# Performance work log

Hardware: AMD Instinct MI355X
Metric: run time of the kernel (lower is better)

Reference implementation:

```python
import jax, jax.numpy as jnp
import numpy as np

EPS = 1e-12  # torch F.normalize eps


def _l2norm(x, axis):
    n = jnp.maximum(jnp.linalg.norm(x, axis=axis, keepdims=True), EPS)
    return x / n


def setup_inputs() -> dict:
    key = jax.random.key(0)
    k1, k2, k3, k4, k5 = jax.random.split(key, 5)
    N, E, IN_DIM, FAC_K, DIM_K = 100000, 1600000, 64, 4, 16
    all_emb = jax.random.normal(k1, (N, IN_DIM), dtype=jnp.float32) * 0.1
    W = jax.random.normal(k2, (FAC_K, IN_DIM, DIM_K), dtype=jnp.float32) * (1.0 / np.sqrt(IN_DIM))
    b = jax.random.normal(k3, (FAC_K, 1, DIM_K), dtype=jnp.float32) * 0.02
    row = jax.random.randint(k4, (E,), 0, N, dtype=jnp.int32)
    col = jax.random.randint(k5, (E,), 0, N, dtype=jnp.int32)
    return {"all_emb": all_emb, "W": W, "b": b, "row": row, "col": col, "iter_k": 2}


def reference(all_emb, W, b, row, col, iter_k):
    N = all_emb.shape[0]
    # factorized projection: [N, in_dim] x [K, in_dim, dk] -> [K, N, dk]
    fac = jnp.einsum('nd,kdf->knf', all_emb, W + b)
    fac = jax.nn.leaky_relu(fac, negative_slope=0.2)
    fac = _l2norm(fac, axis=2)

    new_fac = fac
    for _ in range(iter_k):
        head = new_fac[:, row]            # [K, E, dk]
        tail = fac[:, col]                # [K, E, dk]
        p_uv = jnp.sum(head * tail, axis=2)   # [K, E]
        p_uv = jax.nn.softmax(p_uv, axis=0)   # softmax over factors
        p_uv = jax.lax.stop_gradient(p_uv)    # original detaches attention
        msg = p_uv[:, :, None] * tail         # [K, E, dk]
        agg = jax.vmap(lambda m: jax.ops.segment_sum(m, row, num_segments=N))(msg)
        new_fac = _l2norm(fac + agg, axis=2)  # [K, N, dk]

    # torch.cat(list(new_fac_emb), dim=1) -> [N, K*dk]
    out = jnp.transpose(new_fac, (1, 0, 2)).reshape(N, -1)
    return out
```

## Files before the change

kernel.cpp:

```cpp
#include <hip/hip_runtime.h>

#define IN_DIM 64
#define FAC_K  4
#define DIM_K  16
#define SH     6
#define EPB    8192
#define CAP    2048

typedef _Float16 h2v __attribute__((ext_vector_type(2)));
typedef _Float16 h8v __attribute__((ext_vector_type(8)));
typedef float    f4v __attribute__((ext_vector_type(4)));

__device__ inline int   h2i(h2v v) { return __builtin_bit_cast(int, v); }
__device__ inline h2v   i2h(int v) { return __builtin_bit_cast(h2v, v); }
__device__ inline h2v   pkh(float a, float b) {
    return __builtin_bit_cast(h2v, __builtin_amdgcn_cvt_pkrtz(a, b));
}

#if __has_builtin(__builtin_amdgcn_fdot2)
__device__ inline float FDOT2(h2v a, h2v b, float c) {
    return __builtin_amdgcn_fdot2(a, b, c, false);
}
#else
__device__ inline float FDOT2(h2v a, h2v b, float c) {
    return c + (float)a.x * (float)b.x + (float)a.y * (float)b.y;
}
#endif

union H8U { h8v v; h2v p[4]; };

#define TSZ 1344

__global__ __launch_bounds__(256) void fac_hist_kernel(
    const float* __restrict__ emb, const float* __restrict__ W,
    const float* __restrict__ b,   _Float16* __restrict__ fac16,
    const int* __restrict__ row,   int* __restrict__ H,
    int N, int E, int FB, int NB_blk, int NBUK)
{
    __shared__ float lds_pool[4 * TSZ];
    const int tid = threadIdx.x;

    if (blockIdx.x >= FB) {
        int* hist = (int*)lds_pool;
        const int hb   = blockIdx.x - FB;
        const int base = hb * EPB;
        for (int i = tid; i < NBUK; i += 256) hist[i] = 0;
        __syncthreads();
#pragma unroll
        for (int i = 0; i < EPB / 256; ++i) {
            int e = base + i * 256 + tid;
            if (e < E) atomicAdd(&hist[row[e] >> SH], 1);
        }
        __syncthreads();
        for (int i = tid; i < NBUK; i += 256)
            H[(size_t)i * NB_blk + hb] = hist[i];
        return;
    }

    const int lane = tid & 63;
    const int l    = lane & 15;
    const int q    = lane >> 4;
    float* T = lds_pool + (tid >> 6) * TSZ;

    H8U Bf[4][2];
#pragma unroll
    for (int t = 0; t < 4; ++t) {
        const float bv = b[16 * t + l];
#pragma unroll
        for (int s = 0; s < 2; ++s) {
            const float* wp = W + t * 1024 + (32 * s + 8 * q) * 16 + l;
#pragma unroll
            for (int jp = 0; jp < 4; ++jp) {
                float w0 = wp[(2 * jp)     * 16] + bv;
                float w1 = wp[(2 * jp + 1) * 16] + bv;
                Bf[t][s].p[jp] = pkh(w0, w1);
            }
        }
    }

    const int ntiles = (N + 15) >> 4;
    const int nw     = FB * 4;
    const int wid    = (blockIdx.x * 256 + tid) >> 6;

    for (int tile = wid; tile < ntiles; tile += nw) {
        const int n0 = tile << 4;
        int nm = n0 + l; if (nm >= N) nm = N - 1;

        f4v acc[4];
#pragma unroll
        for (int t = 0; t < 4; ++t) acc[t] = f4v{0.f, 0.f, 0.f, 0.f};

#pragma unroll
        for (int s = 0; s < 2; ++s) {
            const float4* ap = (const float4*)(emb + (size_t)nm * 64 + 32 * s + 8 * q);
            float4 a0 = ap[0], a1 = ap[1];
            H8U A;
            A.p[0] = pkh(a0.x, a0.y); A.p[1] = pkh(a0.z, a0.w);
            A.p[2] = pkh(a1.x, a1.y); A.p[3] = pkh(a1.z, a1.w);
#pragma unroll
            for (int t = 0; t < 4; ++t)
                acc[t] = __builtin_amdgcn_mfma_f32_16x16x32_f16(A.v, Bf[t][s].v, acc[t], 0, 0, 0);
        }

#pragma unroll
        for (int t = 0; t < 4; ++t) {
            f4v v = acc[t];
            f4v vr;
#pragma unroll
            for (int r = 0; r < 4; ++r)
                vr[r] = fmaxf(v[r], 0.f) + 0.2f * fminf(v[r], 0.f);
            const int o = 16 * t + l;
            ((f4v*)(T + 20 * o + 16 * t + 4 * q))[0] = vr;
        }
        float vv[16];
        float ss = 0.f;
#pragma unroll
        for (int i = 0; i < 16; ++i) {
            float x = T[20 * (16 * q + i) + 16 * q + l];
            vv[i] = x;
            ss = fmaf(x, x, ss);
        }
        float inv = 1.0f / fmaxf(sqrtf(ss), 1e-12f);
        H8U o0, o1;
#pragma unroll
        for (int jp = 0; jp < 4; ++jp) {
            o0.p[jp] = pkh(vv[2 * jp]     * inv, vv[2 * jp + 1] * inv);
            o1.p[jp] = pkh(vv[8 + 2 * jp] * inv, vv[9 + 2 * jp] * inv);
        }
        if (n0 + l < N) {
            uint4* dst = (uint4*)(fac16 + (size_t)(n0 + l) * 64 + q * 16);
            dst[0] = __builtin_bit_cast(uint4, o0.v);
            dst[1] = __builtin_bit_cast(uint4, o1.v);
        }
    }
}

__global__ __launch_bounds__(1024) void scan1_kernel(
    const int* __restrict__ in, int* __restrict__ out,
    int* __restrict__ bsum, int M)
{
    __shared__ int wsum[16];
    const int tid  = threadIdx.x;
    const int lane = tid & 63;
    const int w    = tid >> 6;
    const int gi   = blockIdx.x * 1024 + tid;

    int sc = (gi < M) ? in[gi] : 0;
#pragma unroll
    for (int d = 1; d < 64; d <<= 1) {
        int y = __shfl_up(sc, d);
        if (lane >= d) sc += y;
    }
    if (lane == 63) wsum[w] = sc;
    __syncthreads();
    if (w == 0) {
        int v = (lane < 16) ? wsum[lane] : 0;
#pragma unroll
        for (int d = 1; d < 16; d <<= 1) {
            int y = __shfl_up(v, d);
            if (lane >= d) v += y;
        }
        if (lane < 16) wsum[lane] = v;
    }
    __syncthreads();
    if (w > 0) sc += wsum[w - 1];
    if (gi < M) out[gi + 1] = sc;
    if (tid == 1023) bsum[blockIdx.x] = sc;
    if (blockIdx.x == 0 && tid == 0) out[0] = 0;
}

__global__ __launch_bounds__(1024) void scan2_kernel(int* __restrict__ bsum, int nb)
{
    __shared__ int sm[1024];
    const int tid = threadIdx.x;
    sm[tid] = (tid < nb) ? bsum[tid] : 0;
    __syncthreads();
    for (int d = 1; d < 1024; d <<= 1) {
        int t = (tid >= d) ? sm[tid - d] : 0;
        __syncthreads();
        sm[tid] += t;
        __syncthreads();
    }
    if (tid < nb) bsum[tid] = (tid > 0) ? sm[tid - 1] : 0;
}

__global__ __launch_bounds__(256) void scatter1_kernel(
    const int* __restrict__ row, const int* __restrict__ col,
    const int* __restrict__ Hscan, const int* __restrict__ bsum,
    int* __restrict__ tmp, int E, int NB_blk, int NBUK)
{
    __shared__ int cur[2048];
    const int tid = threadIdx.x;
    const int jb  = blockIdx.x;
    const int base = jb * EPB;
    for (int i = tid; i < NBUK; i += 256) {
        int g = i * NB_blk + jb;
        int v = Hscan[g];
        if (g >= 1) v += bsum[(g - 1) >> 10];
        cur[i] = v;
    }
    __syncthreads();
#pragma unroll
    for (int it = 0; it < EPB / 256; ++it) {
        int e = base + it * 256 + tid;
        if (e < E) {
            int r = row[e];
            int pos = atomicAdd(&cur[r >> SH], 1);
            tmp[pos] = ((r & 63) << 17) | col[e];
        }
    }
}

__global__ __launch_bounds__(256, 8) void agg_kernel(
    const _Float16* __restrict__ fac16, const int* __restrict__ tmp,
    const int* __restrict__ Hscan, const int* __restrict__ bsum,
    float* __restrict__ nf_out, int E, int NB_blk, int NBUK, int N)
{
    __shared__ int csr[CAP];
    __shared__ int hist[64];
    __shared__ int curx[64];
    __shared__ int offl[65];

    const int tid = threadIdx.x;
    const int b   = blockIdx.x;

    const int g0 = b * NB_blk;
    const int gE = g0 + NB_blk;
    const int start = Hscan[g0] + (g0 >= 1 ? bsum[(g0 - 1) >> 10] : 0);
    const int end   = Hscan[gE] + bsum[(gE - 1) >> 10];
    const int cnt   = end - start;
    const bool fits = (cnt <= CAP);

    if (tid < 64) hist[tid] = 0;
    __syncthreads();
    if (fits) {
        for (int i = tid; i < cnt; i += 256)
            atomicAdd(&hist[tmp[start + i] >> 17], 1);
        __syncthreads();
        if (tid < 64) {
            int e = hist[tid];
            int sc = e;
#pragma unroll
            for (int d = 1; d < 64; d <<= 1) {
                int y = __shfl_up(sc, d);
                if (tid >= d) sc += y;
            }
            int ex = sc - e;
            offl[tid] = ex;
            curx[tid] = ex;
            if (tid == 63) offl[64] = sc;
        }
        __syncthreads();
        for (int i = tid; i < cnt; i += 256) {
            int u = tmp[start + i];
            int pos = atomicAdd(&curx[u >> 17], 1);
            csr[pos] = u & 0x1FFFF;
        }
    }
    __syncthreads();

    const int grp = tid >> 4;
    const int k   = tid & 3;
    const int q   = (tid >> 2) & 3;

    for (int round = 0; round < 4; ++round) {
        const int lr = round * 16 + grp;
        const int n  = (b << SH) + lr;
        if (n >= N) continue;

        const _Float16* frow = fac16 + (size_t)n * 64 + k * 16;
        uint4 fa = ((const uint4*)frow)[0];
        uint4 fb = ((const uint4*)frow)[1];
        h2v fh[8] = { i2h(fa.x), i2h(fa.y), i2h(fa.z), i2h(fa.w),
                      i2h(fb.x), i2h(fb.y), i2h(fb.z), i2h(fb.w) };
        float f32[16];
#pragma unroll
        for (int r = 0; r < 8; ++r) { f32[2*r] = (float)fh[r].x; f32[2*r+1] = (float)fh[r].y; }
        h2v hh[8];
#pragma unroll
        for (int r = 0; r < 8; ++r) hh[r] = fh[r];

        int s_l = 0, len = 0;
        if (fits) { s_l = offl[lr]; len = offl[lr + 1] - s_l; }

        float vv[16];
#pragma unroll 1
        for (int pass = 0; pass < 2; ++pass) {
            h2v acc2[8];
#pragma unroll
            for (int r = 0; r < 8; ++r) acc2[r] = h2v{(_Float16)0.f, (_Float16)0.f};

            if (fits) {
                if (len > 0) {
                    int e0 = (q < len) ? q : len - 1;
                    const uint4* tp0 = (const uint4*)(fac16 + (size_t)csr[s_l + e0] * 64 + k * 16);
                    uint4 ta0 = tp0[0], tb0 = tp0[1];
                    uint4 ta1 = ta0, tb1 = tb0;
                    if (len > 4) {
                        int e1 = (4 + q < len) ? 4 + q : len - 1;
                        const uint4* tp1 = (const uint4*)(fac16 + (size_t)csr[s_l + e1] * 64 + k * 16);
                        ta1 = tp1[0]; tb1 = tp1[1];
                    }
                    for (int i = 0; i < len; i += 4) {
                        uint4 a = ta0, bb2 = tb0;
                        ta0 = ta1; tb0 = tb1;
                        const bool valid = (i + q) < len;
                        if (i + 8 < len) {
                            int e2 = (i + 8 + q < len) ? i + 8 + q : len - 1;
                            const uint4* tp2 = (const uint4*)(fac16 + (size_t)csr[s_l + e2] * 64 + k * 16);
                            ta1 = tp2[0]; tb1 = tp2[1];
                        }
                        h2v t2[8] = { i2h(a.x), i2h(a.y), i2h(a.z), i2h(a.w),
                                      i2h(bb2.x), i2h(bb2.y), i2h(bb2.z), i2h(bb2.w) };
                        float p = 0.f;
#pragma unroll
                        for (int r = 0; r < 8; ++r) p = FDOT2(hh[r], t2[r], p);
                        float exv = valid ? __expf(p) : 0.f;
                        float qs = exv + __shfl_xor(exv, 1);
                        qs += __shfl_xor(qs, 2);
                        float w = valid ? exv * __builtin_amdgcn_rcpf(qs) : 0.f;
                        _Float16 wh = (_Float16)w;
                        h2v w2; w2.x = wh; w2.y = wh;
#pragma unroll
                        for (int r = 0; r < 8; ++r) acc2[r] += w2 * t2[r];
                    }
                }
            } else {
                for (int i = 0; i < cnt; ++i) {
                    int u = tmp[start + i];
                    if ((u >> 17) != lr) continue;
                    int cc = u & 0x1FFFF;
                    const uint4* tp = (const uint4*)(fac16 + (size_t)cc * 64 + k * 16);
                    uint4 a = tp[0], bb2 = tp[1];
                    h2v t2[8] = { i2h(a.x), i2h(a.y), i2h(a.z), i2h(a.w),
                                  i2h(bb2.x), i2h(bb2.y), i2h(bb2.z), i2h(bb2.w) };
                    float p = 0.f;
#pragma unroll
                    for (int r = 0; r < 8; ++r) p = FDOT2(hh[r], t2[r], p);
                    float exv = __expf(p);
                    float qs = exv + __shfl_xor(exv, 1);
                    qs += __shfl_xor(qs, 2);
                    float w = (q == 0) ? exv * __builtin_amdgcn_rcpf(qs) : 0.f;
                    _Float16 wh = (_Float16)w;
                    h2v w2; w2.x = wh; w2.y = wh;
#pragma unroll
                    for (int r = 0; r < 8; ++r) acc2[r] += w2 * t2[r];
                }
            }

#pragma unroll
            for (int r = 0; r < 8; ++r) {
                acc2[r] += i2h(__shfl_xor(h2i(acc2[r]), 4));
                acc2[r] += i2h(__shfl_xor(h2i(acc2[r]), 8));
            }
            float ss = 0.f;
#pragma unroll
            for (int r = 0; r < 8; ++r) {
                vv[2*r]   = f32[2*r]   + (float)acc2[r].x;
                vv[2*r+1] = f32[2*r+1] + (float)acc2[r].y;
            }
#pragma unroll
            for (int d = 0; d < 16; ++d) ss = fmaf(vv[d], vv[d], ss);
            float inv = 1.0f / fmaxf(sqrtf(ss), 1e-12f);
#pragma unroll
            for (int d = 0; d < 16; ++d) vv[d] *= inv;
            if (pass == 0) {
#pragma unroll
                for (int r = 0; r < 8; ++r) {
                    h2v t; t.x = (_Float16)vv[2*r]; t.y = (_Float16)vv[2*r+1];
                    hh[r] = t;
                }
            }
        }

        float4 o;
        o.x = (q==0) ? vv[0]  : (q==1) ? vv[4]  : (q==2) ? vv[8]  : vv[12];
        o.y = (q==0) ? vv[1]  : (q==1) ? vv[5]  : (q==2) ? vv[9]  : vv[13];
        o.z = (q==0) ? vv[2]  : (q==1) ? vv[6]  : (q==2) ? vv[10] : vv[14];
        o.w = (q==0) ? vv[3]  : (q==1) ? vv[7]  : (q==2) ? vv[11] : vv[15];
        ((float4*)(nf_out + (size_t)n * 64 + k * 16))[q] = o;
    }
}

extern "C" void kernel_launch(void* const* d_in, const int* in_sizes, int n_in,
                              void* d_out, int out_size, void* d_ws, size_t ws_size,
                              hipStream_t stream) {
    const float* emb = (const float*)d_in[0];
    const float* W   = (const float*)d_in[1];
    const float* b   = (const float*)d_in[2];
    const int*   row = (const int*)d_in[3];
    const int*   col = (const int*)d_in[4];

    const int N = in_sizes[0] / IN_DIM;
    const int E = in_sizes[3];

    const int NBUK   = (N + 63) >> SH;
    const int NB_blk = (E + EPB - 1) / EPB;
    const int M      = NBUK * NB_blk;

    float* nf = (float*)d_out;

    _Float16* fac16 = (_Float16*)d_ws;
    int*      tmp   = (int*)(fac16 + (size_t)N * 64);
    int*      H     = tmp + E;
    int*      Hscan = H + M;
    int*      bsum  = Hscan + (M + 1);

    const int nb1 = (M + 1023) / 1024;
    const int FB  = 512;

    fac_hist_kernel<<<FB + NB_blk, 256, 0, stream>>>(
        emb, W, b, fac16, row, H, N, E, FB, NB_blk, NBUK);
    scan1_kernel<<<nb1, 1024, 0, stream>>>(H, Hscan, bsum, M);
    scan2_kernel<<<1, 1024, 0, stream>>>(bsum, nb1);
    scatter1_kernel<<<NB_blk, 256, 0, stream>>>(row, col, Hscan, bsum, tmp, E, NB_blk, NBUK);
    agg_kernel<<<NBUK, 256, 0, stream>>>(fac16, tmp, Hscan, bsum, nf, E, NB_blk, NBUK, N);
}
```

Measured before the change: 226.5 us.

## Split each aggregation bucket across two blocks and use DPP quad reductions

Each 64-row bucket in the aggregation kernel is now processed by two blocks that each own 32 destination rows, doubling grid size and lowering per-block work and LDS use. Edges are repacked to store the precomputed byte offset of the tail row, removing index multiplication in the gather loop. Softmax sums over the four factor lanes use DPP quad permutes instead of generic shuffles. The split means each block scans the whole bucket's edge list, so that read traffic is duplicated.

```diff
diff --git a/kernel.cpp b/kernel.cpp
--- a/kernel.cpp
+++ b/kernel.cpp
@@ -5,7 +5,7 @@
 #define DIM_K  16
 #define SH     6
 #define EPB    8192
-#define CAP    2048
+#define CAP    1536
 
 typedef _Float16 h2v __attribute__((ext_vector_type(2)));
 typedef _Float16 h8v __attribute__((ext_vector_type(8)));
@@ -26,6 +26,15 @@
     return c + (float)a.x * (float)b.x + (float)a.y * (float)b.y;
 }
 #endif
+
+__device__ inline float qadd_xor1(float x) {
+    int y = __builtin_amdgcn_update_dpp(0, __builtin_bit_cast(int, x), 0xB1, 0xF, 0xF, true);
+    return x + __builtin_bit_cast(float, y);
+}
+__device__ inline float qadd_xor2(float x) {
+    int y = __builtin_amdgcn_update_dpp(0, __builtin_bit_cast(int, x), 0x4E, 0xF, 0xF, true);
+    return x + __builtin_bit_cast(float, y);
+}
 
 union H8U { h8v v; h2v p[4]; };
 
@@ -206,7 +215,7 @@
         if (e < E) {
             int r = row[e];
             int pos = atomicAdd(&cur[r >> SH], 1);
-            tmp[pos] = ((r & 63) << 17) | col[e];
+            tmp[pos] = ((r & 63) << 24) | (col[e] << 7);
         }
     }
 }
@@ -217,44 +226,50 @@
     float* __restrict__ nf_out, int E, int NB_blk, int NBUK, int N)
 {
     __shared__ int csr[CAP];
-    __shared__ int hist[64];
-    __shared__ int curx[64];
-    __shared__ int offl[65];
-
-    const int tid = threadIdx.x;
-    const int b   = blockIdx.x;
+    __shared__ int hist[32];
+    __shared__ int curx[32];
+    __shared__ int offl[33];
+
+    const int tid  = threadIdx.x;
+    const int b    = blockIdx.x >> 1;
+    const int half = blockIdx.x & 1;
 
     const int g0 = b * NB_blk;
     const int gE = g0 + NB_blk;
     const int start = Hscan[g0] + (g0 >= 1 ? bsum[(g0 - 1) >> 10] : 0);
     const int end   = Hscan[gE] + bsum[(gE - 1) >> 10];
     const int cnt   = end - start;
-    const bool fits = (cnt <= CAP);
-
-    if (tid < 64) hist[tid] = 0;
-    __syncthreads();
+
+    if (tid < 32) hist[tid] = 0;
+    __syncthreads();
+    for (int i = tid; i < cnt; i += 256) {
+        int rl = tmp[start + i] >> 24;
+        if ((rl >> 5) == half) atomicAdd(&hist[rl & 31], 1);
+    }
+    __syncthreads();
+    if (tid < 32) {
+        int e = hist[tid];
+        int sc = e;
+#pragma unroll
+        for (int d = 1; d < 32; d <<= 1) {
+            int y = __shfl_up(sc, d);
+            if (tid >= d) sc += y;
+        }
+        int ex = sc - e;
+        offl[tid] = ex;
+        curx[tid] = ex;
+        if (tid == 31) offl[32] = sc;
+    }
+    __syncthreads();
+    const bool fits = (offl[32] <= CAP);
     if (fits) {
-        for (int i = tid; i < cnt; i += 256)
-            atomicAdd(&hist[tmp[start + i] >> 17], 1);
-        __syncthreads();
-        if (tid < 64) {
-            int e = hist[tid];
-            int sc = e;
-#pragma unroll
-            for (int d = 1; d < 64; d <<= 1) {
-                int y = __shfl_up(sc, d);
-                if (tid >= d) sc += y;
-            }
-            int ex = sc - e;
-            offl[tid] = ex;
-            curx[tid] = ex;
-            if (tid == 63) offl[64] = sc;
-        }
-        __syncthreads();
         for (int i = tid; i < cnt; i += 256) {
             int u = tmp[start + i];
-            int pos = atomicAdd(&curx[u >> 17], 1);
-            csr[pos] = u & 0x1FFFF;
+            int rl = u >> 24;
+            if ((rl >> 5) == half) {
+                int pos = atomicAdd(&curx[rl & 31], 1);
+                csr[pos] = u & 0xFFFFFF;
+            }
         }
     }
     __syncthreads();
@@ -262,10 +277,12 @@
     const int grp = tid >> 4;
     const int k   = tid & 3;
     const int q   = (tid >> 2) & 3;
-
-    for (int round = 0; round < 4; ++round) {
+    const char* facB = (const char*)fac16;
+    const int   kb   = k * 32;
+
+    for (int round = 0; round < 2; ++round) {
         const int lr = round * 16 + grp;
-        const int n  = (b << SH) + lr;
+        const int n  = (b << SH) + (half << 5) + lr;
         if (n >= N) continue;
 
         const _Float16* frow = fac16 + (size_t)n * 64 + k * 16;
@@ -293,12 +310,12 @@
             if (fits) {
                 if (len > 0) {
                     int e0 = (q < len) ? q : len - 1;
-                    const uint4* tp0 = (const uint4*)(fac16 + (size_t)csr[s_l + e0] * 64 + k * 16);
+                    const uint4* tp0 = (const uint4*)(facB + csr[s_l + e0] + kb);
                     uint4 ta0 = tp0[0], tb0 = tp0[1];
                     uint4 ta1 = ta0, tb1 = tb0;
                     if (len > 4) {
                         int e1 = (4 + q < len) ? 4 + q : len - 1;
-                        const uint4* tp1 = (const uint4*)(fac16 + (size_t)csr[s_l + e1] * 64 + k * 16);
+                        const uint4* tp1 = (const uint4*)(facB + csr[s_l + e1] + kb);
                         ta1 = tp1[0]; tb1 = tp1[1];
                     }
                     for (int i = 0; i < len; i += 4) {
@@ -307,7 +324,7 @@
                         const bool valid = (i + q) < len;
                         if (i + 8 < len) {
                             int e2 = (i + 8 + q < len) ? i + 8 + q : len - 1;
-                            const uint4* tp2 = (const uint4*)(fac16 + (size_t)csr[s_l + e2] * 64 + k * 16);
+                            const uint4* tp2 = (const uint4*)(facB + csr[s_l + e2] + kb);
                             ta1 = tp2[0]; tb1 = tp2[1];
                         }
                         h2v t2[8] = { i2h(a.x), i2h(a.y), i2h(a.z), i2h(a.w),
@@ -316,8 +333,8 @@
 #pragma unroll
                         for (int r = 0; r < 8; ++r) p = FDOT2(hh[r], t2[r], p);
                         float exv = valid ? __expf(p) : 0.f;
-                        float qs = exv + __shfl_xor(exv, 1);
-                        qs += __shfl_xor(qs, 2);
+                        float qs = qadd_xor1(exv);
+                        qs = qadd_xor2(qs);
                         float w = valid ? exv * __builtin_amdgcn_rcpf(qs) : 0.f;
                         _Float16 wh = (_Float16)w;
                         h2v w2; w2.x = wh; w2.y = wh;
@@ -326,11 +343,11 @@
                     }
                 }
             } else {
+                const int want = (half << 5) | lr;
                 for (int i = 0; i < cnt; ++i) {
                     int u = tmp[start + i];
-                    if ((u >> 17) != lr) continue;
-                    int cc = u & 0x1FFFF;
-                    const uint4* tp = (const uint4*)(fac16 + (size_t)cc * 64 + k * 16);
+                    if ((u >> 24) != want) continue;
+                    const uint4* tp = (const uint4*)(facB + (u & 0xFFFFFF) + kb);
                     uint4 a = tp[0], bb2 = tp[1];
                     h2v t2[8] = { i2h(a.x), i2h(a.y), i2h(a.z), i2h(a.w),
                                   i2h(bb2.x), i2h(bb2.y), i2h(bb2.z), i2h(bb2.w) };
@@ -338,8 +355,8 @@
 #pragma unroll
                     for (int r = 0; r < 8; ++r) p = FDOT2(hh[r], t2[r], p);
                     float exv = __expf(p);
-                    float qs = exv + __shfl_xor(exv, 1);
-                    qs += __shfl_xor(qs, 2);
+                    float qs = qadd_xor1(exv);
+                    qs = qadd_xor2(qs);
                     float w = (q == 0) ? exv * __builtin_amdgcn_rcpf(qs) : 0.f;
                     _Float16 wh = (_Float16)w;
                     h2v w2; w2.x = wh; w2.y = wh;
@@ -414,5 +431,5 @@
     scan1_kernel<<<nb1, 1024, 0, stream>>>(H, Hscan, bsum, M);
     scan2_kernel<<<1, 1024, 0, stream>>>(bsum, nb1);
     scatter1_kernel<<<NB_blk, 256, 0, stream>>>(row, col, Hscan, bsum, tmp, E, NB_blk, NBUK);
-    agg_kernel<<<NBUK, 256, 0, stream>>>(fac16, tmp, Hscan, bsum, nf, E, NB_blk, NBUK, N);
-}
+    agg_kernel<<<NBUK * 2, 256, 0, stream>>>(fac16, tmp, Hscan, bsum, nf, E, NB_blk, NBUK, N);
+}
```

Measured after the change: 210.0 us. 7.3% less time.
